# Optimization experiments

Measured on AMD Instinct MI355X. Metric: run time of the kernel, lower is better.

## Reference

```python
import jax, jax.numpy as jnp
import numpy as np

N = 100000   # nodes
E = 1600000  # edges
F_IN = 128
H = 128
C = 20


def setup_inputs() -> dict:
    key = jax.random.key(0)
    ks = jax.random.split(key, 12)
    s = lambda k, sh: jax.random.normal(k, sh, dtype=jnp.float32) * 0.05
    return {
        "x": jax.random.normal(ks[0], (N, F_IN), dtype=jnp.float32),
        "edge_index": jax.random.randint(ks[1], (2, E), 0, N, dtype=jnp.int64),
        # SAGEConv1: lin_l (neighbor, with bias), lin_r (root, no bias)
        "W1l": s(ks[2], (H, F_IN)), "b1": jnp.zeros((H,), jnp.float32), "W1r": s(ks[3], (H, F_IN)),
        # SAGEConv2
        "W2l": s(ks[4], (H, H)), "b2": jnp.zeros((H,), jnp.float32), "W2r": s(ks[5], (H, H)),
        # MLP head
        "Wm1": s(ks[6], (H, H)), "bm1": jnp.zeros((H,), jnp.float32),
        "Wm2": s(ks[7], (C, H)), "bm2": jnp.zeros((C,), jnp.float32),
    }


def _sage_conv(x, src, dst, Wl, bl, Wr):
    # PyG SAGEConv (aggr='mean'): out = lin_l(mean_{j in N(i)} x_j) + lin_r(x_i)
    msg = x[src]                                             # [E, d] irregular gather
    agg = jax.ops.segment_sum(msg, dst, num_segments=N)      # [N, d] scatter-add
    cnt = jax.ops.segment_sum(jnp.ones((msg.shape[0], 1), x.dtype), dst, num_segments=N)
    mean = agg / jnp.maximum(cnt, 1.0)
    return mean @ Wl.T + bl + x @ Wr.T


def reference(x, edge_index, W1l, b1, W1r, W2l, b2, W2r, Wm1, bm1, Wm2, bm2):
    src, dst = edge_index[0], edge_index[1]
    # two SAGEConv layers, each followed by relu (dropout = identity at eval)
    h = jax.nn.relu(_sage_conv(x, src, dst, W1l, b1, W1r))
    h = jax.nn.relu(_sage_conv(h, src, dst, W2l, b2, W2r))
    # MLP: Linear -> dropout(identity) -> ReLU -> Linear, then sigmoid
    h = jax.nn.relu(h @ Wm1.T + bm1)
    return jax.nn.sigmoid(h @ Wm2.T + bm2)
```

## Files before the change

kernel.cpp:

```cpp
#include <hip/hip_runtime.h>
#include <math.h>

#define NODES 100000
#define EDGES 1600000
#define HF 128
#define NC 20
#define CAPN 64
#define EPB 4096
#define NSB ((EDGES + EPB - 1) / EPB)
#define XB ((NODES * HF / 8 + 255) / 256)

typedef __attribute__((ext_vector_type(8))) short bf16x8;
typedef __attribute__((ext_vector_type(4))) float f32x4;
typedef __attribute__((ext_vector_type(2))) float f32x2;

__device__ __forceinline__ ushort f2b(float f) {
    uint u = __float_as_uint(f);
    uint r = (u + 0x7FFFu + ((u >> 16) & 1u)) >> 16;
    return (ushort)r;
}
__device__ __forceinline__ uchar f2q(float f) {
    return (uchar)(__builtin_amdgcn_cvt_pk_fp8_f32(f, f, 0, false) & 0xFF);
}

__global__ void prep_kernel(const float* __restrict__ x, ushort* __restrict__ xb,
                            uchar* __restrict__ xq,
                            const float* __restrict__ a, const float* __restrict__ b,
                            const float* __restrict__ c, const float* __restrict__ d,
                            const float* __restrict__ e, const float* __restrict__ wm2,
                            ushort* __restrict__ wb,
                            const int* __restrict__ src, const int* __restrict__ dst,
                            int* __restrict__ cnt, int* __restrict__ ssrcp,
                            int n8, int E) {
    int blk = blockIdx.x;
    int t = threadIdx.x;
    if (blk < NSB) {
        int base = blk * EPB;
        for (int i = t; i < EPB; i += 256) {
            int ee = base + i;
            if (ee < E) {
                int dd = dst[ee];
                int slot = atomicAdd(&cnt[dd], 1);
                if (slot < CAPN)
                    ssrcp[(size_t)dd * CAPN + slot] = src[ee];
            }
        }
    } else if (blk < NSB + XB) {
        int i = (blk - NSB) * 256 + t;
        if (i >= n8) return;
        const float4* p = (const float4*)x + (size_t)i * 2;
        float4 va = p[0], vb = p[1];
        uint4 o;
        o.x = (uint)f2b(va.x) | ((uint)f2b(va.y) << 16);
        o.y = (uint)f2b(va.z) | ((uint)f2b(va.w) << 16);
        o.z = (uint)f2b(vb.x) | ((uint)f2b(vb.y) << 16);
        o.w = (uint)f2b(vb.z) | ((uint)f2b(vb.w) << 16);
        ((uint4*)xb)[i] = o;
        uint2 q;
        q.x = __builtin_amdgcn_cvt_pk_fp8_f32(va.x, va.y, 0, false);
        q.x = __builtin_amdgcn_cvt_pk_fp8_f32(va.z, va.w, q.x, true);
        q.y = __builtin_amdgcn_cvt_pk_fp8_f32(vb.x, vb.y, 0, false);
        q.y = __builtin_amdgcn_cvt_pk_fp8_f32(vb.z, vb.w, q.y, true);
        ((uint2*)xq)[i] = q;
    } else {
        int i = (blk - NSB - XB) * 256 + t;
        if (i < 81920) {
            const float* srcs[5] = {a, b, c, d, e};
            wb[i] = f2b(srcs[i >> 14][i & 16383]);
        } else if (i < 86016) {
            int j = i - 81920;
            wb[i] = ((j >> 7) < NC) ? f2b(wm2[j]) : (ushort)0;
        }
    }
}

template<bool EMITQ, bool FUSE>
__global__ __launch_bounds__(512)
void fused_sage_layer(const uchar* __restrict__ Xq, const ushort* __restrict__ X,
                      const int* __restrict__ ssrcp, const int* __restrict__ cnt,
                      const ushort* __restrict__ Wl, const ushort* __restrict__ Wr,
                      const float* __restrict__ bias, ushort* __restrict__ out,
                      uchar* __restrict__ outq,
                      const ushort* __restrict__ Wm1b, const ushort* __restrict__ Wm2b,
                      const float* __restrict__ bm1, const float* __restrict__ bm2,
                      float* __restrict__ fout, int n) {
    __shared__ ushort sh[64][136];
    __shared__ int sidx[64 * CAPN];
    __shared__ int s_len[64];
    int row0b = blockIdx.x * 64;
    int t = threadIdx.x;

    if (t < 64) {
        int node = row0b + t;
        s_len[t] = (node < n) ? min(cnt[node], CAPN) : 0;
    }
    int nrows = min(64, n - row0b);
    int lim = nrows * CAPN;
    const int* wsrc = ssrcp + (size_t)row0b * CAPN;
    for (int i = t; i < lim; i += 512) sidx[i] = wsrc[i] << 7;
    __syncthreads();

    {
        int sub = t & 31;
        int sel = sub >> 3;
        int cg = sub & 7;
        const uchar* xc = Xq + cg * 16;
        for (int batch = 0; batch < 4; ++batch) {
            int nloc = batch * 16 + (t >> 5);
            int node = row0b + nloc;
            f32x2 acc2[8];
#pragma unroll
            for (int i = 0; i < 8; ++i) acc2[i] = f32x2{0.f, 0.f};
            int len = s_len[nloc];
            int sbase = nloc * CAPN;

            for (int e = 0; e < len; e += 16) {
                uint4 v[4];
#pragma unroll
                for (int w = 0; w < 4; ++w) {
                    int ee = e + 4 * w + sel;
                    int off = sidx[sbase + ee];
                    uint4 vv = {0u, 0u, 0u, 0u};
                    if (ee < len)
                        vv = *(const uint4*)(xc + (size_t)(uint)off);
                    v[w] = vv;
                }
#pragma unroll
                for (int w = 0; w < 4; ++w) {
                    const uint* pp = (const uint*)&v[w];
#pragma unroll
                    for (int i = 0; i < 4; ++i) {
                        f32x2 lof = __builtin_amdgcn_cvt_pk_f32_fp8(pp[i], false);
                        f32x2 hif = __builtin_amdgcn_cvt_pk_f32_fp8(pp[i], true);
                        acc2[2 * i]     += lof;
                        acc2[2 * i + 1] += hif;
                    }
                }
            }
#pragma unroll
            for (int i = 0; i < 8; ++i) {
                acc2[i].x += __shfl_xor(acc2[i].x, 8);
                acc2[i].x += __shfl_xor(acc2[i].x, 16);
                acc2[i].y += __shfl_xor(acc2[i].y, 8);
                acc2[i].y += __shfl_xor(acc2[i].y, 16);
            }
            if (sel == 0 && node < n) {
                float invd = 1.0f / fmaxf((float)len, 1.0f);
                uint4 o0, o1;
                uint* p0 = (uint*)&o0;
                uint* p1 = (uint*)&o1;
#pragma unroll
                for (int i = 0; i < 4; ++i) {
                    p0[i] = (uint)f2b(acc2[i].x * invd) | ((uint)f2b(acc2[i].y * invd) << 16);
                    p1[i] = (uint)f2b(acc2[4 + i].x * invd) | ((uint)f2b(acc2[4 + i].y * invd) << 16);
                }
                *(uint4*)(&sh[nloc][cg * 16]) = o0;
                *(uint4*)(&sh[nloc][cg * 16 + 8]) = o1;
            }
        }
    }
    __syncthreads();

    int wave = t >> 6;
    int lane = t & 63;
    int m = lane & 15, quad = lane >> 4;
    int col = wave * 16 + m;

    bf16x8 bl[4], br[4];
#pragma unroll
    for (int ks = 0; ks < 4; ++ks) {
        bl[ks] = *(const bf16x8*)(Wl + (size_t)col * HF + ks * 32 + quad * 8);
        br[ks] = *(const bf16x8*)(Wr + (size_t)col * HF + ks * 32 + quad * 8);
    }
    float bia = bias[col];

    if (!FUSE) {
#pragma unroll
        for (int rt = 0; rt < 4; ++rt) {
            int row0 = row0b + rt * 16;
            if (row0 >= n) break;
            f32x4 acc = {0.f, 0.f, 0.f, 0.f};
            const ushort* arow = X + (size_t)(row0 + m) * HF + quad * 8;
#pragma unroll
            for (int ks = 0; ks < 4; ++ks) {
                bf16x8 a = *(const bf16x8*)(&sh[rt * 16 + m][ks * 32 + quad * 8]);
                acc = __builtin_amdgcn_mfma_f32_16x16x32_bf16(a, bl[ks], acc, 0, 0, 0);
                bf16x8 ar = *(const bf16x8*)(arow + ks * 32);
                acc = __builtin_amdgcn_mfma_f32_16x16x32_bf16(ar, br[ks], acc, 0, 0, 0);
            }
#pragma unroll
            for (int i = 0; i < 4; ++i) {
                int r = row0 + quad * 4 + i;
                if (r < n) {
                    float v = fmaxf(acc[i] + bia, 0.f);
                    out[(size_t)r * HF + col] = f2b(v);
                    if (EMITQ) outq[(size_t)r * HF + col] = f2q(v);
                }
            }
        }
    } else {
        f32x4 accs[4];
#pragma unroll
        for (int rt = 0; rt < 4; ++rt) {
            int row0 = row0b + rt * 16;
            f32x4 acc = {0.f, 0.f, 0.f, 0.f};
            if (row0 < n) {
                const ushort* arow = X + (size_t)(row0 + m) * HF + quad * 8;
#pragma unroll
                for (int ks = 0; ks < 4; ++ks) {
                    bf16x8 a = *(const bf16x8*)(&sh[rt * 16 + m][ks * 32 + quad * 8]);
                    acc = __builtin_amdgcn_mfma_f32_16x16x32_bf16(a, bl[ks], acc, 0, 0, 0);
                    bf16x8 ar = *(const bf16x8*)(arow + ks * 32);
                    acc = __builtin_amdgcn_mfma_f32_16x16x32_bf16(ar, br[ks], acc, 0, 0, 0);
                }
            }
            accs[rt] = acc;
        }
        __syncthreads();
#pragma unroll
        for (int rt = 0; rt < 4; ++rt)
#pragma unroll
            for (int i = 0; i < 4; ++i)
                sh[rt * 16 + quad * 4 + i][col] = f2b(fmaxf(accs[rt][i] + bia, 0.f));
        __syncthreads();

        bf16x8 w1[4];
#pragma unroll
        for (int ks = 0; ks < 4; ++ks)
            w1[ks] = *(const bf16x8*)(Wm1b + (size_t)col * HF + ks * 32 + quad * 8);
        float hb = bm1[col];
        f32x4 hacc[4];
#pragma unroll
        for (int rt = 0; rt < 4; ++rt) {
            f32x4 acc = {0.f, 0.f, 0.f, 0.f};
#pragma unroll
            for (int ks = 0; ks < 4; ++ks) {
                bf16x8 a = *(const bf16x8*)(&sh[rt * 16 + m][ks * 32 + quad * 8]);
                acc = __builtin_amdgcn_mfma_f32_16x16x32_bf16(a, w1[ks], acc, 0, 0, 0);
            }
            hacc[rt] = acc;
        }
        __syncthreads();
#pragma unroll
        for (int rt = 0; rt < 4; ++rt)
#pragma unroll
            for (int i = 0; i < 4; ++i)
                sh[rt * 16 + quad * 4 + i][col] = f2b(fmaxf(hacc[rt][i] + hb, 0.f));
        __syncthreads();

        if (wave < 4) {
            bf16x8 c0f[4], c1f[4];
#pragma unroll
            for (int ks = 0; ks < 4; ++ks) {
                c0f[ks] = *(const bf16x8*)(Wm2b + (size_t)m * HF + ks * 32 + quad * 8);
                c1f[ks] = *(const bf16x8*)(Wm2b + (size_t)(16 + m) * HF + ks * 32 + quad * 8);
            }
            f32x4 o0 = {0.f, 0.f, 0.f, 0.f};
            f32x4 o1 = {0.f, 0.f, 0.f, 0.f};
#pragma unroll
            for (int ks = 0; ks < 4; ++ks) {
                bf16x8 a = *(const bf16x8*)(&sh[wave * 16 + m][ks * 32 + quad * 8]);
                o0 = __builtin_amdgcn_mfma_f32_16x16x32_bf16(a, c0f[ks], o0, 0, 0, 0);
                o1 = __builtin_amdgcn_mfma_f32_16x16x32_bf16(a, c1f[ks], o1, 0, 0, 0);
            }
            float bb0 = bm2[m];
            float bb1 = (m < 4) ? bm2[16 + m] : 0.f;
#pragma unroll
            for (int i = 0; i < 4; ++i) {
                int row = row0b + wave * 16 + quad * 4 + i;
                if (row < n) {
                    fout[(size_t)row * NC + m] = 1.0f / (1.0f + expf(-(o0[i] + bb0)));
                    if (m < 4)
                        fout[(size_t)row * NC + 16 + m] = 1.0f / (1.0f + expf(-(o1[i] + bb1)));
                }
            }
        }
    }
}

extern "C" void kernel_launch(void* const* d_in, const int* in_sizes, int n_in,
                              void* d_out, int out_size, void* d_ws, size_t ws_size,
                              hipStream_t stream) {
    const float* x   = (const float*)d_in[0];
    const int*   ei  = (const int*)d_in[1];
    const float* W1l = (const float*)d_in[2];
    const float* b1  = (const float*)d_in[3];
    const float* W1r = (const float*)d_in[4];
    const float* W2l = (const float*)d_in[5];
    const float* b2  = (const float*)d_in[6];
    const float* W2r = (const float*)d_in[7];
    const float* Wm1 = (const float*)d_in[8];
    const float* bm1 = (const float*)d_in[9];
    const float* Wm2 = (const float*)d_in[10];
    const float* bm2 = (const float*)d_in[11];
    float* out = (float*)d_out;

    const int N = NODES, E = EDGES;
    const int* src = ei;
    const int* dst = ei + E;

    int* cnt    = (int*)d_ws;
    int* ssrcp  = cnt + 100352;
    ushort* xb  = (ushort*)(ssrcp + (size_t)N * CAPN);
    ushort* h1  = xb + (size_t)N * HF;
    ushort* wb  = h1 + (size_t)N * HF;
    uchar* xq   = (uchar*)(wb + 86016);
    uchar* h1q  = xq + (size_t)N * HF;
    ushort* wb1l = wb;
    ushort* wb1r = wb + 16384;
    ushort* wb2l = wb + 32768;
    ushort* wb2r = wb + 49152;
    ushort* wbm1 = wb + 65536;
    ushort* wbm2 = wb + 81920;

    const int n8 = N * HF / 8;

    hipMemsetAsync(cnt, 0, N * sizeof(int), stream);
    prep_kernel<<<NSB + XB + 336, 256, 0, stream>>>(
        x, xb, xq, W1l, W1r, W2l, W2r, Wm1, Wm2, wb, src, dst, cnt, ssrcp, n8, E);

    const int fusedBlocks = (N + 63) / 64;

    fused_sage_layer<true, false><<<fusedBlocks, 512, 0, stream>>>(
        xq, xb, ssrcp, cnt, wb1l, wb1r, b1, h1, h1q,
        nullptr, nullptr, nullptr, nullptr, nullptr, N);
    fused_sage_layer<false, true><<<fusedBlocks, 512, 0, stream>>>(
        h1q, h1, ssrcp, cnt, wb2l, wb2r, b2, nullptr, nullptr,
        wbm1, wbm2, bm1, bm2, out, N);
}
```

Baseline: 333.8 us.

## Bucket edges by destination range before building padded neighbor lists

The CSR-like neighbor list build now runs in two passes. First, each block histograms its edges into coarse 256-node buckets in shared memory and scatters (src,dst) pairs into per-bucket regions of a staging buffer that reuses the h1 area. Second, a new csr_build kernel processes one bucket per block and does the per-node atomic slot assignment. The aim is better locality for the scattered global atomics and for writes into ssrcp. In exchange it adds an extra kernel launch and an extra pass over the edge data, and it relies on no bucket exceeding its fixed capacity of 4608 edges; an overflow would not be detected.

```diff
diff --git a/kernel.cpp b/kernel.cpp
--- a/kernel.cpp
+++ b/kernel.cpp
@@ -6,8 +6,12 @@
 #define HF 128
 #define NC 20
 #define CAPN 64
+#define BSHIFT 8
+#define BNODES 256
+#define NBK ((NODES + BNODES - 1) / BNODES)
+#define CAP 4608
 #define EPB 4096
-#define NSB ((EDGES + EPB - 1) / EPB)
+#define NPB ((EDGES + EPB - 1) / EPB)
 #define XB ((NODES * HF / 8 + 255) / 256)
 
 typedef __attribute__((ext_vector_type(8))) short bf16x8;
@@ -30,23 +34,39 @@
                             const float* __restrict__ e, const float* __restrict__ wm2,
                             ushort* __restrict__ wb,
                             const int* __restrict__ src, const int* __restrict__ dst,
-                            int* __restrict__ cnt, int* __restrict__ ssrcp,
+                            int* __restrict__ bcur, uint2* __restrict__ ebuf,
                             int n8, int E) {
+    __shared__ int h[NBK];
+    __shared__ int basea[NBK];
     int blk = blockIdx.x;
     int t = threadIdx.x;
-    if (blk < NSB) {
+    if (blk < NPB) {
         int base = blk * EPB;
+        for (int i = t; i < NBK; i += 256) h[i] = 0;
+        __syncthreads();
+        for (int i = t; i < EPB; i += 256) {
+            int ee = base + i;
+            if (ee < E) atomicAdd(&h[dst[ee] >> BSHIFT], 1);
+        }
+        __syncthreads();
+        for (int i = t; i < NBK; i += 256) {
+            int cc = h[i];
+            basea[i] = cc ? (i * CAP + atomicAdd(&bcur[i], cc)) : 0;
+        }
+        __syncthreads();
+        for (int i = t; i < NBK; i += 256) h[i] = 0;
+        __syncthreads();
         for (int i = t; i < EPB; i += 256) {
             int ee = base + i;
             if (ee < E) {
                 int dd = dst[ee];
-                int slot = atomicAdd(&cnt[dd], 1);
-                if (slot < CAPN)
-                    ssrcp[(size_t)dd * CAPN + slot] = src[ee];
-            }
-        }
-    } else if (blk < NSB + XB) {
-        int i = (blk - NSB) * 256 + t;
+                int bb = dd >> BSHIFT;
+                int pos = basea[bb] + atomicAdd(&h[bb], 1);
+                ebuf[pos] = make_uint2((uint)src[ee], (uint)dd);
+            }
+        }
+    } else if (blk < NPB + XB) {
+        int i = (blk - NPB) * 256 + t;
         if (i >= n8) return;
         const float4* p = (const float4*)x + (size_t)i * 2;
         float4 va = p[0], vb = p[1];
@@ -63,7 +83,7 @@
         q.y = __builtin_amdgcn_cvt_pk_fp8_f32(vb.z, vb.w, q.y, true);
         ((uint2*)xq)[i] = q;
     } else {
-        int i = (blk - NSB - XB) * 256 + t;
+        int i = (blk - NPB - XB) * 256 + t;
         if (i < 81920) {
             const float* srcs[5] = {a, b, c, d, e};
             wb[i] = f2b(srcs[i >> 14][i & 16383]);
@@ -71,6 +91,20 @@
             int j = i - 81920;
             wb[i] = ((j >> 7) < NC) ? f2b(wm2[j]) : (ushort)0;
         }
+    }
+}
+
+__global__ void csr_build(const uint2* __restrict__ ebuf, const int* __restrict__ bcur,
+                          int* __restrict__ cnt, int* __restrict__ ssrcp) {
+    int b = blockIdx.x;
+    int t = threadIdx.x;
+    int e0 = b * CAP;
+    int cnt_b = bcur[b];
+    for (int i = t; i < cnt_b; i += 256) {
+        uint2 ed = ebuf[e0 + i];
+        int slot = atomicAdd(&cnt[ed.y], 1);
+        if (slot < CAPN)
+            ssrcp[(size_t)ed.y * CAPN + slot] = (int)ed.x;
     }
 }
 
@@ -300,9 +334,11 @@
     const int* dst = ei + E;
 
     int* cnt    = (int*)d_ws;
-    int* ssrcp  = cnt + 100352;
+    int* bcur   = cnt + 100352;
+    int* ssrcp  = bcur + 512;
     ushort* xb  = (ushort*)(ssrcp + (size_t)N * CAPN);
     ushort* h1  = xb + (size_t)N * HF;
+    uint2* ebuf = (uint2*)h1;
     ushort* wb  = h1 + (size_t)N * HF;
     uchar* xq   = (uchar*)(wb + 86016);
     uchar* h1q  = xq + (size_t)N * HF;
@@ -315,9 +351,10 @@
 
     const int n8 = N * HF / 8;
 
-    hipMemsetAsync(cnt, 0, N * sizeof(int), stream);
-    prep_kernel<<<NSB + XB + 336, 256, 0, stream>>>(
-        x, xb, xq, W1l, W1r, W2l, W2r, Wm1, Wm2, wb, src, dst, cnt, ssrcp, n8, E);
+    hipMemsetAsync(cnt, 0, (100352 + 512) * sizeof(int), stream);
+    prep_kernel<<<NPB + XB + 336, 256, 0, stream>>>(
+        x, xb, xq, W1l, W1r, W2l, W2r, Wm1, Wm2, wb, src, dst, bcur, ebuf, n8, E);
+    csr_build<<<NBK, 256, 0, stream>>>(ebuf, bcur, cnt, ssrcp);
 
     const int fusedBlocks = (N + 63) / 64;
 
```

Measured after the change: 330.6 us. Within noise of the previous version (-0.9%).
